# Optimization experiments

Measured on AMD Instinct MI355X. Metric: run time of the kernel, lower is better.

## Reference

```python
import jax, jax.numpy as jnp
from jax import lax
import numpy as np

B, N, P, NB = 64, 16, 20, 30      # frames, boxes/frame, num_persons, num_behaviors
C, F, OUT, SR = 1024, 14, 3, 2    # fmap channels, fmap size, roi output, sampling ratio
EPS = 1e-5


def roi_align_one(fmap, boxes):
    """fmap: [C,H,W]; boxes: [K,4]=(x1,y1,x2,y2) in fmap coords. Returns [K,C,OUT,OUT].
    torchvision-style roi_align (aligned=False) with fixed sampling_ratio=SR."""
    H, W = fmap.shape[1], fmap.shape[2]
    x1, y1, x2, y2 = boxes[:, 0], boxes[:, 1], boxes[:, 2], boxes[:, 3]
    rw = jnp.maximum(x2 - x1, 1.0)
    rh = jnp.maximum(y2 - y1, 1.0)
    S = OUT * SR
    pos = (jnp.arange(S, dtype=fmap.dtype) + 0.5) / SR            # sample pos in bin units
    ys = jnp.clip(y1[:, None] + pos[None, :] * (rh / OUT)[:, None], 0.0, H - 1.0)  # [K,S]
    xs = jnp.clip(x1[:, None] + pos[None, :] * (rw / OUT)[:, None], 0.0, W - 1.0)
    y0 = jnp.floor(ys); x0 = jnp.floor(xs)
    y0i = y0.astype(jnp.int32); x0i = x0.astype(jnp.int32)
    y1i = jnp.minimum(y0i + 1, H - 1); x1i = jnp.minimum(x0i + 1, W - 1)
    wy = ys - y0; wx = xs - x0                                     # [K,S]
    g = lambda yi, xi: fmap[:, yi[:, :, None], xi[:, None, :]]     # [C,K,S,S]
    v = (g(y0i, x0i) * ((1 - wy)[:, :, None] * (1 - wx)[:, None, :])
         + g(y0i, x1i) * ((1 - wy)[:, :, None] * wx[:, None, :])
         + g(y1i, x0i) * (wy[:, :, None] * (1 - wx)[:, None, :])
         + g(y1i, x1i) * (wy[:, :, None] * wx[:, None, :]))
    v = jnp.transpose(v, (1, 0, 2, 3))                             # [K,C,S,S]
    K = boxes.shape[0]
    return v.reshape(K, C, OUT, SR, OUT, SR).mean(axis=(3, 5))     # avg over samples


roi_align = jax.vmap(roi_align_one, in_axes=(0, 0))


def bn(x, g, b, m, v):
    s = (g / jnp.sqrt(v + EPS))[None, :, None, None]
    return x * s + (b - m * g / jnp.sqrt(v + EPS))[None, :, None, None]


def leaky(x):
    return jnp.where(x > 0, x, 0.1 * x)


def behavior_conv(x, w1, g1, b1, m1, v1, w2, g2, b2, m2, v2):
    dn = ('NCHW', 'OIHW', 'NCHW')
    x = lax.conv_general_dilated(x, w1, (1, 1), 'SAME', dimension_numbers=dn)
    x = leaky(bn(x, g1, b1, m1, v1))
    x = lax.conv_general_dilated(x, w2, (1, 1), 'SAME', dimension_numbers=dn)
    return leaky(bn(x, g2, b2, m2, v2))


def forward(fmap, boxes, conv1_w, bn1_g, bn1_b, bn1_m, bn1_v,
            conv2_w, bn2_g, bn2_b, bn2_m, bn2_v,
            conv1d_w, conv1d_b, fc1_w, fc1_b, fc2_w, fc2_b, person_idx):
    # --- global feature: ROI over the whole fmap per frame ---
    gbox = jnp.broadcast_to(jnp.array([[0.0, 0.0, F, F]], jnp.float32), (B, 1, 4))
    g_roi = roi_align(fmap, gbox).reshape(B, C, OUT, OUT)          # [B,1024,3,3]
    g_feat = behavior_conv(g_roi, conv1_w, bn1_g, bn1_b, bn1_m, bn1_v,
                           conv2_w, bn2_g, bn2_b, bn2_m, bn2_v)    # [B,256,3,3]
    g_feat = g_feat.reshape(B, 256 * OUT * OUT)                    # [B,2304]

    # --- per-box ROI features ---
    i_roi = roi_align(fmap, boxes).reshape(B * N, C, OUT, OUT)     # [B*N,1024,3,3]
    i_feat = behavior_conv(i_roi, conv1_w, bn1_g, bn1_b, bn1_m, bn1_v,
                           conv2_w, bn2_g, bn2_b, bn2_m, bn2_v)
    i_feat = i_feat.reshape(B, N, 256 * OUT * OUT)                 # [B,N,2304]

    # --- scatter-accumulate into behavior tensor [B,P,2304] ---
    behavior = jnp.broadcast_to(g_feat[:, None, :], (B, P, 2304))
    bidx = jnp.broadcast_to(jnp.arange(B)[:, None], (B, N))
    behavior = behavior.at[bidx, person_idx].add(i_feat)

    # --- temporal conv1d across the batch axis for every person slot ---
    x = jnp.transpose(behavior, (1, 2, 0))                         # [P,2304,B]
    x = lax.conv_general_dilated(x, conv1d_w, (1,), 'SAME',
                                 dimension_numbers=('NCH', 'OIH', 'NCH'))
    x = x + conv1d_b[None, :, None]                                # [P,2304,B]

    # --- gather each (frame, box)'s person feature at its frame and classify ---
    x = jnp.transpose(x, (2, 0, 1))                                # [B,P,2304]
    feats = jnp.take_along_axis(x, person_idx[:, :, None], axis=1) # [B,N,2304]
    h = jax.nn.relu(feats @ fc1_w + fc1_b)                         # dropout off (eval)
    return h @ fc2_w + fc2_b                                       # [B,N,NB]


def setup_inputs() -> dict:
    key = jax.random.key(0)
    ks = jax.random.split(key, 16)
    fmap = jax.random.normal(ks[0], (B, C, F, F), jnp.float32)
    lo = jax.random.uniform(ks[1], (B, N, 2), jnp.float32, 0.0, 9.0)
    sz = jax.random.uniform(ks[2], (B, N, 2), jnp.float32, 2.0, 5.0)
    hi = jnp.minimum(lo + sz, float(F))
    boxes = jnp.concatenate([lo, hi], axis=-1)                     # (x1,y1,x2,y2)
    person_idx = jax.random.randint(ks[3], (B, N), 0, P)
    s = lambda k, shape, fan: jax.random.normal(k, shape, jnp.float32) / np.sqrt(fan)
    return {
        'fmap': fmap, 'boxes': boxes, 'person_idx': person_idx,
        'conv1_w': s(ks[4], (512, 1024, 3, 3), 1024 * 9),
        'bn1_g': jnp.ones(512), 'bn1_b': jnp.zeros(512),
        'bn1_m': jnp.zeros(512), 'bn1_v': jnp.ones(512),
        'conv2_w': s(ks[5], (256, 512, 3, 3), 512 * 9),
        'bn2_g': jnp.ones(256), 'bn2_b': jnp.zeros(256),
        'bn2_m': jnp.zeros(256), 'bn2_v': jnp.ones(256),
        'conv1d_w': s(ks[6], (2304, 2304, 3), 2304 * 3),
        'conv1d_b': jnp.zeros(2304),
        'fc1_w': s(ks[7], (2304, 1024), 2304), 'fc1_b': jnp.zeros(1024),
        'fc2_w': s(ks[8], (1024, NB), 1024), 'fc2_b': jnp.zeros(NB),
    }


def reference(fmap, boxes, person_idx, conv1_w, bn1_g, bn1_b, bn1_m, bn1_v,
              conv2_w, bn2_g, bn2_b, bn2_m, bn2_v,
              conv1d_w, conv1d_b, fc1_w, fc1_b, fc2_w, fc2_b):
    return forward(fmap, boxes, conv1_w, bn1_g, bn1_b, bn1_m, bn1_v,
                   conv2_w, bn2_g, bn2_b, bn2_m, bn2_v,
                   conv1d_w, conv1d_b, fc1_w, fc1_b, fc2_w, fc2_b, person_idx)
```

## Files before the change

### kernel.cpp

```cpp
#include <hip/hip_runtime.h>
#include <hip/hip_bf16.h>
#include <cstdint>
#include <cstddef>

typedef __bf16 bf16;
typedef __bf16 bf16x8 __attribute__((ext_vector_type(8)));
typedef float f32x4 __attribute__((ext_vector_type(4)));

__device__ __forceinline__ void gload_lds16(const bf16* g, bf16* l) {
    __builtin_amdgcn_global_load_lds((const __attribute__((address_space(1))) void*)g,
                                     (__attribute__((address_space(3))) void*)l, 16, 0, 0);
}

template <int NT>
__global__ void __launch_bounds__(256) repack_w(const float* __restrict__ w, bf16* __restrict__ out,
                                                int OC, int IC) {
    int idx = blockIdx.x * 256 + threadIdx.x;
    if (idx >= OC * IC) return;
    int oc = idx / IC;
    int ic = idx - oc * IC;
    const float* src = w + (size_t)idx * NT;
    #pragma unroll
    for (int t = 0; t < NT; t++)
        out[(size_t)oc * NT * IC + t * IC + ic] = (bf16)src[t];
}

__global__ void __launch_bounds__(256) transpose_fc1(const float* __restrict__ w, bf16* __restrict__ out) {
    __shared__ float t[32][33];
    int iT = blockIdx.x * 32;
    int oT = blockIdx.y * 32;
    int tx = threadIdx.x, ty = threadIdx.y;
    #pragma unroll
    for (int j = 0; j < 4; j++)
        t[ty + j * 8][tx] = w[(size_t)(iT + ty + j * 8) * 1024 + oT + tx];
    __syncthreads();
    #pragma unroll
    for (int j = 0; j < 4; j++)
        out[(size_t)(oT + ty + j * 8) * 2304 + iT + tx] = (bf16)t[tx][ty + j * 8];
}

__global__ void __launch_bounds__(256) setup_all(int* __restrict__ rb1t, int* __restrict__ rb2t,
                                                 int* __restrict__ rb1dg, int* __restrict__ rbid,
                                                 const int* __restrict__ pidx,
                                                 bf16* __restrict__ zp1, bf16* __restrict__ zp2,
                                                 bf16* __restrict__ zp3,
                                                 const float* g1, const float* b1, const float* m1, const float* v1,
                                                 const float* g2, const float* b2, const float* m2, const float* v2,
                                                 float* __restrict__ s1, float* __restrict__ t1,
                                                 float* __restrict__ s2, float* __restrict__ t2,
                                                 const float* __restrict__ fc2_w, bf16* __restrict__ w2t) {
    int m = blockIdx.x * 256 + threadIdx.x;
    if (m < 9 * 9856) {
        int tap = m / 9856, r = m - tap * 9856;
        int mm = r < 9792 ? r : 0;
        int img = mm / 9, pos = mm - img * 9;
        int oy = pos / 3, ox = pos - oy * 3;
        int ty = tap / 3, tx = tap - ty * 3;
        int iy = oy + ty - 1, ix = ox + tx - 1;
        bool valid = (iy >= 0) & (iy < 3) & (ix >= 0) & (ix < 3);
        int cell = img * 9 + iy * 3 + ix;
        rb1t[m] = valid ? 1024 + cell * 1024 : 0;
        rb2t[m] = valid ? 512 + cell * 512 : 0;
    }
    if (m < 3 * 1024) {
        int tap = m / 1024, r = m - tap * 1024;
        int b = r >> 4;
        int p = pidx[r];
        int tt = b + tap - 1;
        bool valid = (tt >= 0) & (tt < 64);
        rb1dg[m] = valid ? 2304 + (p * 64 + tt) * 2304 : 0;
    }
    if (m < 1024) rbid[m] = m * 2304;
    if (m < 30 * 1024) {
        int n = m / 1024, k = m - n * 1024;
        w2t[m] = (bf16)fc2_w[(size_t)k * 30 + n];
    }
    if (m < 1024) zp1[m] = (bf16)0.f;
    if (m < 512)  zp2[m] = (bf16)0.f;
    if (m < 2304) zp3[m] = (bf16)0.f;
    if (m < 512) {
        float sc = g1[m] * rsqrtf(v1[m] + 1e-5f);
        s1[m] = sc; t1[m] = b1[m] - m1[m] * sc;
    } else if (m < 768) {
        int i = m - 512;
        float sc = g2[i] * rsqrtf(v2[i] + 1e-5f);
        s2[i] = sc; t2[i] = b2[i] - m2[i] * sc;
    }
}

__global__ void __launch_bounds__(256) transpose_fmap(const float* __restrict__ fmap, bf16* __restrict__ fml) {
    __shared__ float t[32][33];
    int img = blockIdx.z;
    int hwT = blockIdx.x * 32;
    int cT  = blockIdx.y * 32;
    int tx = threadIdx.x, ty = threadIdx.y;
    #pragma unroll
    for (int j = 0; j < 4; j++) {
        int c = cT + ty + j * 8;
        int hw = hwT + tx;
        if (hw < 196)
            t[ty + j * 8][tx] = fmap[((size_t)img * 1024 + c) * 196 + hw];
    }
    __syncthreads();
    #pragma unroll
    for (int j = 0; j < 4; j++) {
        int hw = hwT + ty + j * 8;
        int c = cT + tx;
        if (hw < 196)
            fml[((size_t)img * 196 + hw) * 1024 + c] = (bf16)t[tx][ty + j * 8];
    }
}

__global__ void __launch_bounds__(128) roi_kernel2(const bf16* __restrict__ fml, const float* __restrict__ boxes,
                                                   bf16* __restrict__ a1c) {
    int box = blockIdx.x;
    int tid = threadIdx.x;
    float x1, y1, x2, y2;
    int img;
    if (box < 64) { img = box; x1 = 0.f; y1 = 0.f; x2 = 14.f; y2 = 14.f; }
    else {
        int ib = box - 64;
        img = ib >> 4;
        const float* bb = boxes + (size_t)ib * 4;
        x1 = bb[0]; y1 = bb[1]; x2 = bb[2]; y2 = bb[3];
    }
    float rw = fmaxf(x2 - x1, 1.f), rh = fmaxf(y2 - y1, 1.f);
    __shared__ float swy[6], swx[6];
    __shared__ int sy0[6], sx0[6];
    if (tid < 6) {
        int i = tid;
        float pos = ((float)i + 0.5f) * 0.5f;
        float yv = fminf(fmaxf(y1 + pos * (rh * (1.f / 3.f)), 0.f), 13.f);
        float y0 = floorf(yv);
        sy0[i] = (int)y0; swy[i] = yv - y0;
        float xv = fminf(fmaxf(x1 + pos * (rw * (1.f / 3.f)), 0.f), 13.f);
        float x0 = floorf(xv);
        sx0[i] = (int)x0; swx[i] = xv - x0;
    }
    __syncthreads();
    const bf16* base = fml + (size_t)img * 196 * 1024 + tid * 8;
    #pragma unroll
    for (int oy = 0; oy < 3; oy++) {
        #pragma unroll
        for (int ox = 0; ox < 3; ox++) {
            float acc[8];
            #pragma unroll
            for (int e = 0; e < 8; e++) acc[e] = 0.f;
            #pragma unroll
            for (int dy = 0; dy < 2; dy++) {
                int sy = 2 * oy + dy;
                int y0 = sy0[sy]; float wy = swy[sy];
                int y1i = min(y0 + 1, 13);
                #pragma unroll
                for (int dx = 0; dx < 2; dx++) {
                    int sx = 2 * ox + dx;
                    int x0 = sx0[sx]; float wx = swx[sx];
                    int x1i = min(x0 + 1, 13);
                    bf16x8 f00 = *(const bf16x8*)(base + (size_t)(y0 * 14 + x0) * 1024);
                    bf16x8 f01 = *(const bf16x8*)(base + (size_t)(y0 * 14 + x1i) * 1024);
                    bf16x8 f10 = *(const bf16x8*)(base + (size_t)(y1i * 14 + x0) * 1024);
                    bf16x8 f11 = *(const bf16x8*)(base + (size_t)(y1i * 14 + x1i) * 1024);
                    float w00 = (1.f - wy) * (1.f - wx), w01 = (1.f - wy) * wx;
                    float w10 = wy * (1.f - wx),         w11 = wy * wx;
                    #pragma unroll
                    for (int e = 0; e < 8; e++)
                        acc[e] += w00 * (float)f00[e] + w01 * (float)f01[e]
                                + w10 * (float)f10[e] + w11 * (float)f11[e];
                }
            }
            bf16x8 o;
            #pragma unroll
            for (int e = 0; e < 8; e++) o[e] = (bf16)(acc[e] * 0.25f);
            *(bf16x8*)(a1c + 1024 + ((size_t)box * 9 + oy * 3 + ox) * 1024 + tid * 8) = o;
        }
    }
}

__global__ void __launch_bounds__(256) assemble(const float* __restrict__ feat, const int* __restrict__ pidx,
                                                bf16* __restrict__ asm3) {
    int b = blockIdx.x;
    int p = blockIdx.y;
    __shared__ int idxs[16];
    if (threadIdx.x < 16) idxs[threadIdx.x] = pidx[b * 16 + threadIdx.x];
    __syncthreads();
    const float* g = feat + (size_t)b * 2304;
    for (int f = threadIdx.x; f < 2304; f += 256) {
        float v = g[f];
        #pragma unroll
        for (int n = 0; n < 16; n++)
            if (idxs[n] == p) v += feat[(size_t)(64 + b * 16 + n) * 2304 + f];
        asm3[2304 + ((size_t)p * 64 + b) * 2304 + f] = (bf16)v;
    }
}

template <int MODE, int NSPLIT>
__global__ void __launch_bounds__(256) gemm_k(const bf16* __restrict__ A, const int* __restrict__ rowtab,
                                              const bf16* __restrict__ Bw, float* __restrict__ outp) {
    constexpr int K   = MODE == 0 ? 9216 : MODE == 1 ? 4608 : MODE == 2 ? 6912 : 2304;
    constexpr int N   = MODE == 0 ? 512  : MODE == 1 ? 256  : MODE == 2 ? 2304 : 1024;
    constexpr int Cin = MODE == 0 ? 1024 : MODE == 1 ? 512  : 2304;
    constexpr int M   = MODE <= 1 ? 9792 : 1024;
    constexpr int MT  = MODE <= 1 ? 9856 : 1024;
    constexpr bool MPAD = (M % 128) != 0;
    constexpr int KTS = (K / 64) / NSPLIT;

    const int bm = blockIdx.y * 128;
    const int bn = blockIdx.x * 128;
    const int z  = blockIdx.z;
    const int tid = threadIdx.x;
    const int lane = tid & 63, wave = tid >> 6;
    const int q = lane >> 4, ln16 = lane & 15;
    const int wr = wave >> 1, wc = wave & 1;

    __shared__ __align__(16) bf16 As[128 * 64];
    __shared__ __align__(16) bf16 Bs[128 * 64];

    const int sr = lane >> 3;
    const int sc = ((lane & 7) ^ sr) * 8;
    const bf16* gB[4];
    #pragma unroll
    for (int u = 0; u < 4; u++)
        gB[u] = Bw + (size_t)(bn + wave * 32 + u * 8 + sr) * K + sc;

    f32x4 acc[4][4];
    #pragma unroll
    for (int mt = 0; mt < 4; mt++)
        #pragma unroll
        for (int nt = 0; nt < 4; nt++)
            acc[mt][nt] = (f32x4){0.f, 0.f, 0.f, 0.f};

    int rbA[4];
    int curtap = -1;
    for (int kt = z * KTS; kt < z * KTS + KTS; kt++) {
        const int k0 = kt * 64;
        const int tap = k0 / Cin;
        const int inner = k0 - tap * Cin;
        if (tap != curtap) {
            curtap = tap;
            #pragma unroll
            for (int u = 0; u < 4; u++)
                rbA[u] = rowtab[tap * MT + bm + wave * 32 + u * 8 + sr];
        }
        const int aoff = inner + sc;

        __syncthreads();
        #pragma unroll
        for (int u = 0; u < 4; u++)
            gload_lds16(A + (size_t)(rbA[u] + aoff), As + (wave * 32 + u * 8) * 64);
        #pragma unroll
        for (int u = 0; u < 4; u++)
            gload_lds16(gB[u] + k0, Bs + (wave * 32 + u * 8) * 64);
        __syncthreads();

        #pragma unroll
        for (int s = 0; s < 2; s++) {
            bf16x8 af[4], bfr[4];
            #pragma unroll
            for (int mt = 0; mt < 4; mt++) {
                int r = wr * 64 + mt * 16 + ln16;
                af[mt] = *(const bf16x8*)(As + r * 64 + (((4 * s + q) ^ (ln16 & 7)) << 3));
            }
            #pragma unroll
            for (int nt = 0; nt < 4; nt++) {
                int r = wc * 64 + nt * 16 + ln16;
                bfr[nt] = *(const bf16x8*)(Bs + r * 64 + (((4 * s + q) ^ (ln16 & 7)) << 3));
            }
            #pragma unroll
            for (int mt = 0; mt < 4; mt++)
                #pragma unroll
                for (int nt = 0; nt < 4; nt++)
                    acc[mt][nt] = __builtin_amdgcn_mfma_f32_16x16x32_bf16(af[mt], bfr[nt], acc[mt][nt], 0, 0, 0);
        }
    }

    #pragma unroll
    for (int mt = 0; mt < 4; mt++) {
        int gmBase = bm + wr * 64 + mt * 16 + q * 4;
        #pragma unroll
        for (int r = 0; r < 4; r++) {
            int gm = gmBase + r;
            if (MPAD && gm >= M) continue;
            #pragma unroll
            for (int nt = 0; nt < 4; nt++) {
                int gn = bn + wc * 64 + nt * 16 + ln16;
                outp[((size_t)z * M + gm) * N + gn] = acc[mt][nt][r];
            }
        }
    }
}

__global__ void __launch_bounds__(256) reduce0_tiled(const float* __restrict__ part,
                                                     float* __restrict__ feat,
                                                     const float* __restrict__ s2, const float* __restrict__ t2) {
    int c = blockIdx.x;
    int t = threadIdx.x;
    float acc[9];
    #pragma unroll
    for (int r = 0; r < 9; r++) acc[r] = 0.f;
    #pragma unroll
    for (int z = 0; z < 6; z++) {
        const float* base = part + ((size_t)z * 9792 + c * 9) * 256 + t;
        #pragma unroll
        for (int r = 0; r < 9; r++) acc[r] += base[r * 256];
    }
    float s = s2[t], b = t2[t];
    __shared__ float L[9 * 257];
    #pragma unroll
    for (int r = 0; r < 9; r++) {
        float v = acc[r] * s + b;
        v = v > 0.f ? v : 0.1f * v;
        L[r * 257 + t] = v;
    }
    __syncthreads();
    float* fout = feat + (size_t)c * 2304;
    #pragma unroll
    for (int k = 0; k < 9; k++) {
        int f = t + k * 256;
        int oc = f / 9, pos = f - oc * 9;
        fout[f] = L[pos * 257 + oc];
    }
}

template <int RMODE>
__global__ void __launch_bounds__(256) reduce_k(const float* __restrict__ part, void* __restrict__ outp,
                                                const float* __restrict__ c0, const float* __restrict__ c1) {
    constexpr int M = RMODE == 1 ? 1024 : RMODE == 2 ? 1024 : 9792;
    constexpr int N = RMODE == 1 ? 2304 : RMODE == 2 ? 1024 : 512;
    constexpr int S = RMODE == 1 ? 4    : RMODE == 2 ? 6    : 3;
    int idx = blockIdx.x * 256 + threadIdx.x;
    if (idx >= M * N) return;
    int m = idx / N, n = idx - m * N;
    float v = 0.f;
    #pragma unroll
    for (int s = 0; s < S; s++) v += part[(size_t)s * M * N + idx];
    if constexpr (RMODE == 1) {
        v += c0[n];
        ((bf16*)outp)[idx] = (bf16)v;
    } else if constexpr (RMODE == 2) {
        v = fmaxf(v + c0[n], 0.f);
        ((bf16*)outp)[idx] = (bf16)v;
    } else {
        v = v * c0[n] + c1[n];
        v = v > 0.f ? v : 0.1f * v;
        ((bf16*)outp)[512 + (size_t)m * 512 + n] = (bf16)v;
    }
}

__global__ void __launch_bounds__(256) fc2_kernel(const bf16* __restrict__ h, const bf16* __restrict__ w2t,
                                                  const float* __restrict__ b2, float* __restrict__ out) {
    int tid = threadIdx.x;
    int m = blockIdx.x * 8 + (tid >> 5);
    int n = tid & 31;
    int n2 = n < 30 ? n : 29;
    const bf16* hr = h + (size_t)m * 1024;
    const bf16* wr = w2t + (size_t)n2 * 1024;
    float acc = 0.f;
    for (int k = 0; k < 1024; k += 8) {
        bf16x8 hv = *(const bf16x8*)(hr + k);
        bf16x8 wv = *(const bf16x8*)(wr + k);
        #pragma unroll
        for (int e = 0; e < 8; e++) acc += (float)hv[e] * (float)wv[e];
    }
    if (n < 30) out[(size_t)m * 30 + n] = acc + b2[n];
}

extern "C" void kernel_launch(void* const* d_in, const int* in_sizes, int n_in,
                              void* d_out, int out_size, void* d_ws, size_t ws_size,
                              hipStream_t stream) {
    const float* fmap     = (const float*)d_in[0];
    const float* boxes    = (const float*)d_in[1];
    const int*   pidx     = (const int*)d_in[2];
    const float* conv1_w  = (const float*)d_in[3];
    const float* bn1_g    = (const float*)d_in[4];
    const float* bn1_b    = (const float*)d_in[5];
    const float* bn1_m    = (const float*)d_in[6];
    const float* bn1_v    = (const float*)d_in[7];
    const float* conv2_w  = (const float*)d_in[8];
    const float* bn2_g    = (const float*)d_in[9];
    const float* bn2_b    = (const float*)d_in[10];
    const float* bn2_m    = (const float*)d_in[11];
    const float* bn2_v    = (const float*)d_in[12];
    const float* conv1d_w = (const float*)d_in[13];
    const float* conv1d_b = (const float*)d_in[14];
    const float* fc1_w    = (const float*)d_in[15];
    const float* fc1_b    = (const float*)d_in[16];
    const float* fc2_w    = (const float*)d_in[17];
    const float* fc2_b    = (const float*)d_in[18];
    float* out = (float*)d_out;

    char* ws = (char*)d_ws;

    float* s1    = (float*)(ws + 0);
    float* t1    = (float*)(ws + 2048);
    float* s2    = (float*)(ws + 4096);
    float* t2    = (float*)(ws + 5120);
    int*   rbid  = (int*)(ws + 6144);
    int*   rb1dg = (int*)(ws + 10240);
    int*   rb1t  = (int*)(ws + 25600);
    int*   rb2t  = (int*)(ws + 380416);
    bf16*  fml    = (bf16*)(ws + 768000);
    float* part1  = (float*)(ws + 768000);
    float* part2  = (float*)(ws + 768000);
    float* part1d = (float*)(ws + 768000);
    float* partfc = (float*)(ws + 768000);
    bf16*  a1c    = (bf16*)(ws + 60930048);
    bf16*  wb1d   = (bf16*)(ws + 60930048);
    bf16*  fc1t   = (bf16*)(ws + 92780544);
    bf16*  xbuf   = (bf16*)(ws + 97499136);
    bf16*  hbuf   = (bf16*)(ws + 102217728);
    bf16*  w2t    = (bf16*)(ws + 104314880);
    bf16*  wb1    = (bf16*)(ws + 104857600);
    bf16*  wb2    = (bf16*)(ws + 114294784);
    bf16*  a2c    = (bf16*)(ws + 116654080);
    bf16*  asm3   = (bf16*)(ws + 126682112);
    float* feat   = (float*)(ws + 132584960);

    bf16* zp1 = a1c;
    bf16* zp2 = a2c;
    bf16* zp3 = asm3;

    setup_all<<<(9 * 9856 + 255) / 256, 256, 0, stream>>>(rb1t, rb2t, rb1dg, rbid, pidx,
                                                          zp1, zp2, zp3,
                                                          bn1_g, bn1_b, bn1_m, bn1_v,
                                                          bn2_g, bn2_b, bn2_m, bn2_v,
                                                          s1, t1, s2, t2, fc2_w, w2t);
    repack_w<9><<<(512 * 1024 + 255) / 256, 256, 0, stream>>>(conv1_w, wb1, 512, 1024);
    repack_w<9><<<(256 * 512 + 255) / 256, 256, 0, stream>>>(conv2_w, wb2, 256, 512);

    transpose_fmap<<<dim3(7, 32, 64), dim3(32, 8), 0, stream>>>(fmap, fml);
    roi_kernel2<<<1088, 128, 0, stream>>>(fml, boxes, a1c);

    gemm_k<0, 3><<<dim3(4, 77, 3), 256, 0, stream>>>(a1c, rb1t, wb1, part1);
    reduce_k<3><<<(9792 * 512 + 255) / 256, 256, 0, stream>>>(part1, a2c, s1, t1);

    repack_w<3><<<(2304 * 2304 + 255) / 256, 256, 0, stream>>>(conv1d_w, wb1d, 2304, 2304);
    transpose_fc1<<<dim3(72, 32), dim3(32, 8), 0, stream>>>(fc1_w, fc1t);

    gemm_k<1, 6><<<dim3(2, 77, 6), 256, 0, stream>>>(a2c, rb2t, wb2, part2);
    reduce0_tiled<<<1088, 256, 0, stream>>>(part2, feat, s2, t2);
    assemble<<<dim3(64, 20), 256, 0, stream>>>(feat, pidx, asm3);
    gemm_k<2, 4><<<dim3(18, 8, 4), 256, 0, stream>>>(asm3, rb1dg, wb1d, part1d);
    reduce_k<1><<<(1024 * 2304 + 255) / 256, 256, 0, stream>>>(part1d, xbuf, conv1d_b, nullptr);
    gemm_k<3, 6><<<dim3(8, 8, 6), 256, 0, stream>>>(xbuf, rbid, fc1t, partfc);
    reduce_k<2><<<(1024 * 1024 + 255) / 256, 256, 0, stream>>>(partfc, hbuf, fc1_b, nullptr);
    fc2_kernel<<<128, 256, 0, stream>>>(hbuf, w2t, fc2_b, out);
    (void)in_sizes; (void)n_in; (void)out_size; (void)ws_size;
}
```

Measured before the change: 493.2 us.

## Reorder conv GEMM rows by output position and skip zero-padded taps

Measured after the change: 473.2 us. 4.1% less time.

```diff
diff --git a/kernel.cpp b/kernel.cpp
--- a/kernel.cpp
+++ b/kernel.cpp
@@ -41,6 +41,7 @@
 
 __global__ void __launch_bounds__(256) setup_all(int* __restrict__ rb1t, int* __restrict__ rb2t,
                                                  int* __restrict__ rb1dg, int* __restrict__ rbid,
+                                                 int* __restrict__ tapmask,
                                                  const int* __restrict__ pidx,
                                                  bf16* __restrict__ zp1, bf16* __restrict__ zp2,
                                                  bf16* __restrict__ zp3,
@@ -53,14 +54,32 @@
     if (m < 9 * 9856) {
         int tap = m / 9856, r = m - tap * 9856;
         int mm = r < 9792 ? r : 0;
-        int img = mm / 9, pos = mm - img * 9;
+        int pos = mm / 1088, img = mm - pos * 1088;
         int oy = pos / 3, ox = pos - oy * 3;
         int ty = tap / 3, tx = tap - ty * 3;
         int iy = oy + ty - 1, ix = ox + tx - 1;
         bool valid = (iy >= 0) & (iy < 3) & (ix >= 0) & (ix < 3);
-        int cell = img * 9 + iy * 3 + ix;
-        rb1t[m] = valid ? 1024 + cell * 1024 : 0;
-        rb2t[m] = valid ? 512 + cell * 512 : 0;
+        int cell = iy * 3 + ix;
+        rb1t[m] = valid ? 1024 + (img * 9 + cell) * 1024 : 0;
+        rb2t[m] = valid ? 512 + (cell * 1088 + img) * 512 : 0;
+    }
+    if (m < 77) {
+        int lo = (m * 128) / 1088;
+        int hiRow = m * 128 + 127; if (hiRow > 9791) hiRow = 9791;
+        int hi = hiRow / 1088;
+        int msk = 0;
+        for (int pos = lo; pos <= hi; ++pos) {
+            int oy = pos / 3, ox = pos - oy * 3;
+            int ym = oy == 0 ? 6 : (oy == 1 ? 7 : 3);
+            int xm = ox == 0 ? 6 : (ox == 1 ? 7 : 3);
+            #pragma unroll
+            for (int ty = 0; ty < 3; ty++)
+                #pragma unroll
+                for (int tx = 0; tx < 3; tx++)
+                    if (((ym >> ty) & 1) & ((xm >> tx) & 1))
+                        msk |= 1 << (ty * 3 + tx);
+        }
+        tapmask[m] = msk;
     }
     if (m < 3 * 1024) {
         int tap = m / 1024, r = m - tap * 1024;
@@ -195,7 +214,8 @@
 
 template <int MODE, int NSPLIT>
 __global__ void __launch_bounds__(256) gemm_k(const bf16* __restrict__ A, const int* __restrict__ rowtab,
-                                              const bf16* __restrict__ Bw, float* __restrict__ outp) {
+                                              const bf16* __restrict__ Bw, float* __restrict__ outp,
+                                              const int* __restrict__ tapmask) {
     constexpr int K   = MODE == 0 ? 9216 : MODE == 1 ? 4608 : MODE == 2 ? 6912 : 2304;
     constexpr int N   = MODE == 0 ? 512  : MODE == 1 ? 256  : MODE == 2 ? 2304 : 1024;
     constexpr int Cin = MODE == 0 ? 1024 : MODE == 1 ? 512  : 2304;
@@ -229,47 +249,93 @@
         for (int nt = 0; nt < 4; nt++)
             acc[mt][nt] = (f32x4){0.f, 0.f, 0.f, 0.f};
 
-    int rbA[4];
-    int curtap = -1;
-    for (int kt = z * KTS; kt < z * KTS + KTS; kt++) {
-        const int k0 = kt * 64;
-        const int tap = k0 / Cin;
-        const int inner = k0 - tap * Cin;
-        if (tap != curtap) {
-            curtap = tap;
+    if constexpr (MODE <= 1) {
+        const int mask = tapmask[blockIdx.y];
+        int ord = 0;
+        for (int tap = 0; tap < 9; ++tap) {
+            if (!((mask >> tap) & 1)) continue;
+            if ((ord++) % NSPLIT != z) continue;
+            int rbA[4];
             #pragma unroll
             for (int u = 0; u < 4; u++)
                 rbA[u] = rowtab[tap * MT + bm + wave * 32 + u * 8 + sr];
+            for (int kk = 0; kk < Cin / 64; ++kk) {
+                const int aoff = kk * 64 + sc;
+                const int k0 = tap * Cin + kk * 64;
+
+                __syncthreads();
+                #pragma unroll
+                for (int u = 0; u < 4; u++)
+                    gload_lds16(A + (size_t)(rbA[u] + aoff), As + (wave * 32 + u * 8) * 64);
+                #pragma unroll
+                for (int u = 0; u < 4; u++)
+                    gload_lds16(gB[u] + k0, Bs + (wave * 32 + u * 8) * 64);
+                __syncthreads();
+
+                #pragma unroll
+                for (int s = 0; s < 2; s++) {
+                    bf16x8 af[4], bfr[4];
+                    #pragma unroll
+                    for (int mt = 0; mt < 4; mt++) {
+                        int r = wr * 64 + mt * 16 + ln16;
+                        af[mt] = *(const bf16x8*)(As + r * 64 + (((4 * s + q) ^ (ln16 & 7)) << 3));
+                    }
+                    #pragma unroll
+                    for (int nt = 0; nt < 4; nt++) {
+                        int r = wc * 64 + nt * 16 + ln16;
+                        bfr[nt] = *(const bf16x8*)(Bs + r * 64 + (((4 * s + q) ^ (ln16 & 7)) << 3));
+                    }
+                    #pragma unroll
+                    for (int mt = 0; mt < 4; mt++)
+                        #pragma unroll
+                        for (int nt = 0; nt < 4; nt++)
+                            acc[mt][nt] = __builtin_amdgcn_mfma_f32_16x16x32_bf16(af[mt], bfr[nt], acc[mt][nt], 0, 0, 0);
+                }
+            }
         }
-        const int aoff = inner + sc;
-
-        __syncthreads();
-        #pragma unroll
-        for (int u = 0; u < 4; u++)
-            gload_lds16(A + (size_t)(rbA[u] + aoff), As + (wave * 32 + u * 8) * 64);
-        #pragma unroll
-        for (int u = 0; u < 4; u++)
-            gload_lds16(gB[u] + k0, Bs + (wave * 32 + u * 8) * 64);
-        __syncthreads();
-
-        #pragma unroll
-        for (int s = 0; s < 2; s++) {
-            bf16x8 af[4], bfr[4];
-            #pragma unroll
-            for (int mt = 0; mt < 4; mt++) {
-                int r = wr * 64 + mt * 16 + ln16;
-                af[mt] = *(const bf16x8*)(As + r * 64 + (((4 * s + q) ^ (ln16 & 7)) << 3));
+    } else {
+        int rbA[4];
+        int curtap = -1;
+        for (int kt = z * KTS; kt < z * KTS + KTS; kt++) {
+            const int k0 = kt * 64;
+            const int tap = k0 / Cin;
+            const int inner = k0 - tap * Cin;
+            if (tap != curtap) {
+                curtap = tap;
+                #pragma unroll
+                for (int u = 0; u < 4; u++)
+                    rbA[u] = rowtab[tap * MT + bm + wave * 32 + u * 8 + sr];
             }
-            #pragma unroll
-            for (int nt = 0; nt < 4; nt++) {
-                int r = wc * 64 + nt * 16 + ln16;
-                bfr[nt] = *(const bf16x8*)(Bs + r * 64 + (((4 * s + q) ^ (ln16 & 7)) << 3));
+            const int aoff = inner + sc;
+
+            __syncthreads();
+            #pragma unroll
+            for (int u = 0; u < 4; u++)
+                gload_lds16(A + (size_t)(rbA[u] + aoff), As + (wave * 32 + u * 8) * 64);
+            #pragma unroll
+            for (int u = 0; u < 4; u++)
+                gload_lds16(gB[u] + k0, Bs + (wave * 32 + u * 8) * 64);
+            __syncthreads();
+
+            #pragma unroll
+            for (int s = 0; s < 2; s++) {
+                bf16x8 af[4], bfr[4];
+                #pragma unroll
+                for (int mt = 0; mt < 4; mt++) {
+                    int r = wr * 64 + mt * 16 + ln16;
+                    af[mt] = *(const bf16x8*)(As + r * 64 + (((4 * s + q) ^ (ln16 & 7)) << 3));
+                }
+                #pragma unroll
+                for (int nt = 0; nt < 4; nt++) {
+                    int r = wc * 64 + nt * 16 + ln16;
+                    bfr[nt] = *(const bf16x8*)(Bs + r * 64 + (((4 * s + q) ^ (ln16 & 7)) << 3));
+                }
+                #pragma unroll
+                for (int mt = 0; mt < 4; mt++)
+                    #pragma unroll
+                    for (int nt = 0; nt < 4; nt++)
+                        acc[mt][nt] = __builtin_amdgcn_mfma_f32_16x16x32_bf16(af[mt], bfr[nt], acc[mt][nt], 0, 0, 0);
             }
-            #pragma unroll
-            for (int mt = 0; mt < 4; mt++)
-                #pragma unroll
-                for (int nt = 0; nt < 4; nt++)
-                    acc[mt][nt] = __builtin_amdgcn_mfma_f32_16x16x32_bf16(af[mt], bfr[nt], acc[mt][nt], 0, 0, 0);
         }
     }
 
@@ -298,10 +364,10 @@
     #pragma unroll
     for (int r = 0; r < 9; r++) acc[r] = 0.f;
     #pragma unroll
-    for (int z = 0; z < 6; z++) {
-        const float* base = part + ((size_t)z * 9792 + c * 9) * 256 + t;
+    for (int z = 0; z < 3; z++) {
         #pragma unroll
-        for (int r = 0; r < 9; r++) acc[r] += base[r * 256];
+        for (int r = 0; r < 9; r++)
+            acc[r] += part[((size_t)z * 9792 + r * 1088 + c) * 256 + t];
     }
     float s = s2[t], b = t2[t];
     __shared__ float L[9 * 257];
@@ -396,6 +462,7 @@
     float* t2    = (float*)(ws + 5120);
     int*   rbid  = (int*)(ws + 6144);
     int*   rb1dg = (int*)(ws + 10240);
+    int*   tapm  = (int*)(ws + 22528);
     int*   rb1t  = (int*)(ws + 25600);
     int*   rb2t  = (int*)(ws + 380416);
     bf16*  fml    = (bf16*)(ws + 768000);
@@ -419,7 +486,7 @@
     bf16* zp2 = a2c;
     bf16* zp3 = asm3;
 
-    setup_all<<<(9 * 9856 + 255) / 256, 256, 0, stream>>>(rb1t, rb2t, rb1dg, rbid, pidx,
+    setup_all<<<(9 * 9856 + 255) / 256, 256, 0, stream>>>(rb1t, rb2t, rb1dg, rbid, tapm, pidx,
                                                           zp1, zp2, zp3,
                                                           bn1_g, bn1_b, bn1_m, bn1_v,
                                                           bn2_g, bn2_b, bn2_m, bn2_v,
@@ -430,18 +497,18 @@
     transpose_fmap<<<dim3(7, 32, 64), dim3(32, 8), 0, stream>>>(fmap, fml);
     roi_kernel2<<<1088, 128, 0, stream>>>(fml, boxes, a1c);
 
-    gemm_k<0, 3><<<dim3(4, 77, 3), 256, 0, stream>>>(a1c, rb1t, wb1, part1);
+    gemm_k<0, 3><<<dim3(4, 77, 3), 256, 0, stream>>>(a1c, rb1t, wb1, part1, tapm);
     reduce_k<3><<<(9792 * 512 + 255) / 256, 256, 0, stream>>>(part1, a2c, s1, t1);
 
     repack_w<3><<<(2304 * 2304 + 255) / 256, 256, 0, stream>>>(conv1d_w, wb1d, 2304, 2304);
     transpose_fc1<<<dim3(72, 32), dim3(32, 8), 0, stream>>>(fc1_w, fc1t);
 
-    gemm_k<1, 6><<<dim3(2, 77, 6), 256, 0, stream>>>(a2c, rb2t, wb2, part2);
+    gemm_k<1, 3><<<dim3(2, 77, 3), 256, 0, stream>>>(a2c, rb2t, wb2, part2, tapm);
     reduce0_tiled<<<1088, 256, 0, stream>>>(part2, feat, s2, t2);
     assemble<<<dim3(64, 20), 256, 0, stream>>>(feat, pidx, asm3);
-    gemm_k<2, 4><<<dim3(18, 8, 4), 256, 0, stream>>>(asm3, rb1dg, wb1d, part1d);
+    gemm_k<2, 4><<<dim3(18, 8, 4), 256, 0, stream>>>(asm3, rb1dg, wb1d, part1d, tapm);
     reduce_k<1><<<(1024 * 2304 + 255) / 256, 256, 0, stream>>>(part1d, xbuf, conv1d_b, nullptr);
-    gemm_k<3, 6><<<dim3(8, 8, 6), 256, 0, stream>>>(xbuf, rbid, fc1t, partfc);
+    gemm_k<3, 6><<<dim3(8, 8, 6), 256, 0, stream>>>(xbuf, rbid, fc1t, partfc, tapm);
     reduce_k<2><<<(1024 * 1024 + 255) / 256, 256, 0, stream>>>(partfc, hbuf, fc1_b, nullptr);
     fc2_kernel<<<128, 256, 0, stream>>>(hbuf, w2t, fc2_b, out);
     (void)in_sizes; (void)n_in; (void)out_size; (void)ws_size;
```
